# Performance work log

Measured on AMD Instinct MI355X. Metric: run time of the kernel, lower is better.

Reference implementation:

```python
import jax, jax.numpy as jnp
import numpy as np

B, H, T, K = 4, 32, 2048, 64
V = K


def setup_inputs() -> dict:
    key = jax.random.key(0)
    k1, k2, k3, k4, k5 = jax.random.split(key, 5)
    r = jax.random.normal(k1, (B, H, T, K), dtype=jnp.float32)
    k = jax.random.normal(k2, (B, H, T, K), dtype=jnp.float32)
    v = jax.random.normal(k3, (B, H, T, V), dtype=jnp.float32)
    # w is a log-decay; keep it negative so exp(w) in (0,1) and the T-step
    # recurrence is stable (matches real RWKV-6 decay values)
    w = -2.0 * jax.random.uniform(k4, (B, H, T, K), dtype=jnp.float32)
    u = jax.random.normal(k5, (H, K), dtype=jnp.float32)
    initial_state = jnp.zeros((B, H, K, V), dtype=jnp.float32)
    return {"r": r, "k": k, "v": v, "w": w, "u": u, "initial_state": initial_state}


def _rwkv6_scan(r, k, v, w, u, initial_state):
    scale = 1.0
    q = r * scale
    decay = jnp.exp(w)  # [B,H,T,K], matches torch: b_w = exp(w)

    # time-major for scan: [T,B,H,K]
    qT = jnp.moveaxis(q, 2, 0)
    kT = jnp.moveaxis(k, 2, 0)
    vT = jnp.moveaxis(v, 2, 0)
    wT = jnp.moveaxis(decay, 2, 0)

    u_b = u[None, :, :, None]  # [1,H,K,1] broadcast like torch b_u

    def step(h, inp):
        bq, bk, bv, bw = inp  # each [B,H,K] (bv is [B,H,V])
        kv = bk[..., :, None] * bv[..., None, :]          # [B,H,K,V]
        o = jnp.einsum('bhkv,bhk->bhv', h + kv * u_b, bq)  # sum over K
        h = h * bw[..., None] + kv                         # decay-gated update
        return h, o

    final_state, oT = jax.lax.scan(step, initial_state, (qT, kT, vT, wT))
    o = jnp.moveaxis(oT, 0, 2)  # [B,H,T,V]
    return o, final_state


def reference(r, k, v, w, u, initial_state):
    return _rwkv6_scan(r, k, v, w, u, initial_state)
```

## Files before the change

kernel.cpp:

```cpp
#include <hip/hip_runtime.h>
#include <math.h>


#define Bdim 4
#define Hdim 32
#define Tdim 2048
#define Kdim 64
#define Vdim 64
#define NC   32
#define CL   64
#define LP   72

typedef __attribute__((ext_vector_type(8))) short short8;
typedef __attribute__((ext_vector_type(4))) short short4_;
typedef __attribute__((ext_vector_type(4))) float float4_;

__device__ __forceinline__ short f2bf(float x) {
    unsigned u = __float_as_uint(x);
    unsigned r = (u + 0x7FFFu + ((u >> 16) & 1u)) >> 16;
    return (short)r;
}

#define MFMA(a, b, c) __builtin_amdgcn_mfma_f32_16x16x32_bf16(a, b, c, 0, 0, 0)

__device__ __forceinline__ void wg_barrier() {
    __builtin_amdgcn_sched_barrier(0);
    asm volatile("s_waitcnt lgkmcnt(0)");
    __builtin_amdgcn_s_barrier();
    __builtin_amdgcn_sched_barrier(0);
}

__global__ __launch_bounds__(512) void rwkv6_fused(
    const float* __restrict__ rin, const float* __restrict__ kin,
    const float* __restrict__ vin, const float* __restrict__ win,
    const float* __restrict__ uin, const float* __restrict__ init,
    float* __restrict__ oout, float* __restrict__ fin)
{
    __shared__ __attribute__((aligned(16))) short Qh[CL * LP];
    __shared__ __attribute__((aligned(16))) short Kh[CL * LP];
    __shared__ __attribute__((aligned(16))) short KhT[CL * LP];
    __shared__ __attribute__((aligned(16))) short Qt[CL * LP];
    __shared__ __attribute__((aligned(16))) short Am[CL * LP];
    __shared__ __attribute__((aligned(16))) short Vt[32 * LP];
    __shared__ __attribute__((aligned(16))) short Ht[32 * LP];
    __shared__ float bsum[8 * 64];
    __shared__ float Dd[CL];

    const int tid  = threadIdx.x;
    const int wv   = tid >> 6;
    const int lane = tid & 63;
    const int quad = lane >> 4, r = lane & 15;

    const int bid = blockIdx.x;
    const int vh  = bid >> 7;
    const int bh  = bid & 127;
    const int h_idx = bh & (Hdim - 1);

    const int m_s = wv >> 2;
    const int n_s = wv & 3;
    const int k_  = 16 * n_s + r;
    const int i_o = wv >> 1;
    const int n_o = wv & 1;

    const float u_ = uin[h_idx * Kdim + lane];

    const int svrow = tid & 31;
    const int skq   = tid >> 5;

    auto blk_addr = [](const short* buf, int row, int blk) -> const char* {
        const int phys = blk ^ ((row >> 3) & 3);
        return (const char*)buf + row * 144 + phys * 16;
    };

    for (int i = tid; i < CL * LP; i += 512) Am[i] = 0;

    float h[4];
#pragma unroll
    for (int reg = 0; reg < 4; ++reg) {
        const int vloc = 16 * m_s + quad * 4 + reg;
        h[reg] = init[((size_t)bh * Kdim + k_) * Vdim + 32 * vh + vloc];
        const int hb = ((k_ >> 3) ^ ((vloc >> 3) & 3));
        *(short*)((char*)Ht + vloc * 144 + hb * 16 + (k_ & 7) * 2) = f2bf(h[reg]);
    }

    float wl[8], ql[8], kl[8], vls[4];
    {
        const size_t b0 = (size_t)bh * Tdim * Kdim;
#pragma unroll
        for (int tt = 0; tt < 8; ++tt) wl[tt] = win[b0 + (8 * wv + tt) * Kdim + lane];
#pragma unroll
        for (int i = 0; i < 4; ++i)
            vls[i] = vin[b0 + (4 * skq + i) * Kdim + 32 * vh + svrow];
#pragma unroll
        for (int tt = 0; tt < 8; ++tt) ql[tt] = rin[b0 + (8 * wv + tt) * Kdim + lane];
#pragma unroll
        for (int tt = 0; tt < 8; ++tt) kl[tt] = kin[b0 + (8 * wv + tt) * Kdim + lane];
    }

    auto atile = [&](int i, int j) {
        const int trow = 16 * i + r;
        short8 qa0 = *(const short8*)&Qh[trow * LP + quad * 8];
        short8 qa1 = *(const short8*)&Qh[trow * LP + 32 + quad * 8];
        const int srow = 16 * j + r;
        const int sb = (srow >> 3) & 7;
        short8 kb0 = *(const short8*)&Kh[srow * LP + ((quad ^ sb) << 3)];
        short8 kb1 = *(const short8*)&Kh[srow * LP + (((quad + 4) ^ sb) << 3)];
        float4_ acc = {0.f, 0.f, 0.f, 0.f};
        acc = MFMA(qa0, kb0, acc);
        acc = MFMA(qa1, kb1, acc);
#pragma unroll
        for (int reg = 0; reg < 4; ++reg) {
            const int tg = 16 * i + quad * 4 + reg;
            const float val = (tg > srow) ? acc[reg] : ((tg == srow) ? Dd[tg] : 0.f);
            Am[tg * LP + srow] = f2bf(val);
        }
    };

    for (int c = 0; c < NC; ++c) {
        const size_t base = ((size_t)bh * Tdim + (size_t)c * CL) * Kdim;

        float wreg[8];
        float cwl = 0.f;
#pragma unroll
        for (int tt = 0; tt < 8; ++tt) { wreg[tt] = wl[tt]; cwl += wl[tt]; }
        bsum[wv * 64 + lane] = cwl;
        {
            short4_ pack;
#pragma unroll
            for (int i = 0; i < 4; ++i) pack[i] = f2bf(vls[i]);
            const int vb = ((skq >> 1) ^ ((svrow >> 3) & 3));
            *(short4_*)((char*)Vt + svrow * 144 + vb * 16 + (skq & 1) * 8) = pack;
        }
        wg_barrier();

        float b[8];
#pragma unroll
        for (int j = 0; j < 8; ++j) b[j] = bsum[j * 64 + lane];
        float pref = 0.f;
#pragma unroll
        for (int j = 0; j < 8; ++j) if (j < wv) pref += b[j];
        const float Cmid = b[0] + b[1] + b[2] + b[3];
        const float eC = __expf(Cmid);
        float cwrun = pref;
        short8 khrow;
#pragma unroll
        for (int tt = 0; tt < 8; ++tt) {
            const int t = 8 * wv + tt;
            const float cwp = cwrun;
            cwrun += wreg[tt];
            const float e1 = __expf(cwp - Cmid);
            Qh[t * LP + lane] = f2bf(ql[tt] * e1);
            Qt[t * LP + lane] = f2bf(ql[tt] * e1 * eC);
            const float e2 = __expf(Cmid - cwrun);
            const short kv = f2bf(kl[tt] * e2);
            Kh[t * LP + ((((lane >> 3) ^ ((t >> 3) & 7)) << 3) | (lane & 7))] = kv;
            khrow[tt] = kv;
            float d3 = ql[tt] * u_ * kl[tt];
#pragma unroll
            for (int off = 32; off > 0; off >>= 1) d3 += __shfl_xor(d3, off);
            if (lane == 0) Dd[t] = d3;
        }
        {
            const int kb = (wv ^ ((lane >> 3) & 3));
            *(short8*)((char*)KhT + lane * 144 + kb * 16) = khrow;
        }
        if (c + 1 < NC) {
            const size_t nb = base + (size_t)CL * Kdim;
#pragma unroll
            for (int tt = 0; tt < 8; ++tt) wl[tt] = win[nb + (8 * wv + tt) * Kdim + lane];
#pragma unroll
            for (int i = 0; i < 4; ++i)
                vls[i] = vin[nb + (4 * skq + i) * Kdim + 32 * vh + svrow];
#pragma unroll
            for (int tt = 0; tt < 8; ++tt) ql[tt] = rin[nb + (8 * wv + tt) * Kdim + lane];
#pragma unroll
            for (int tt = 0; tt < 8; ++tt) kl[tt] = kin[nb + (8 * wv + tt) * Kdim + lane];
        }
        wg_barrier();

        {
            int i0, j0;
            if (wv == 0)      { i0 = 0; j0 = 0; }
            else if (wv < 3)  { i0 = 1; j0 = wv - 1; }
            else if (wv < 6)  { i0 = 2; j0 = wv - 3; }
            else              { i0 = 3; j0 = wv - 6; }
            atile(i0, j0);
            if (wv < 2) atile(3, 2 + wv);
        }
        wg_barrier();

        {
            const int trow = 16 * i_o + r;
            short8 aa0 = *(const short8*)&Am[trow * LP + quad * 8];
            short8 aa1 = *(const short8*)&Am[trow * LP + 32 + quad * 8];
            short8 qt0 = *(const short8*)&Qt[trow * LP + quad * 8];
            short8 qt1 = *(const short8*)&Qt[trow * LP + 32 + quad * 8];
            const int vrow = 16 * n_o + r;
            short8 vb0 = *(const short8*)blk_addr(Vt, vrow, quad);
            short8 vb1 = *(const short8*)blk_addr(Vt, vrow, quad + 4);
            short8 hb0 = *(const short8*)blk_addr(Ht, vrow, quad);
            short8 hb1 = *(const short8*)blk_addr(Ht, vrow, quad + 4);
            float4_ o4 = {0.f, 0.f, 0.f, 0.f};
            o4 = MFMA(aa0, vb0, o4);
            o4 = MFMA(aa1, vb1, o4);
            o4 = MFMA(qt0, hb0, o4);
            o4 = MFMA(qt1, hb1, o4);
            float* op = oout + base;
#pragma unroll
            for (int reg = 0; reg < 4; ++reg)
                op[(16 * i_o + quad * 4 + reg) * Vdim + 32 * vh + 16 * n_o + r] = o4[reg];
        }

        float4_ sc = {0.f, 0.f, 0.f, 0.f};
        {
            const int vrow = 16 * m_s + r;
            short8 va0 = *(const short8*)blk_addr(Vt, vrow, quad);
            short8 va1 = *(const short8*)blk_addr(Vt, vrow, quad + 4);
            short8 kc0 = *(const short8*)blk_addr(KhT, k_, quad);
            short8 kc1 = *(const short8*)blk_addr(KhT, k_, quad + 4);
            sc = MFMA(va0, kc0, sc);
            sc = MFMA(va1, kc1, sc);
        }
        float totk = 0.f, cmk = 0.f;
#pragma unroll
        for (int j = 0; j < 8; ++j) {
            const float bb = bsum[j * 64 + k_];
            totk += bb;
            if (j < 4) cmk += bb;
        }
        wg_barrier();

        {
            const float eA = __expf(totk);
            const float eS = __expf(totk - cmk);
#pragma unroll
            for (int reg = 0; reg < 4; ++reg) {
                h[reg] = h[reg] * eA + sc[reg] * eS;
                const int vloc = 16 * m_s + quad * 4 + reg;
                const int hb = ((k_ >> 3) ^ ((vloc >> 3) & 3));
                *(short*)((char*)Ht + vloc * 144 + hb * 16 + (k_ & 7) * 2) = f2bf(h[reg]);
            }
        }
    }

#pragma unroll
    for (int reg = 0; reg < 4; ++reg)
        fin[((size_t)bh * Kdim + k_) * Vdim + 32 * vh + 16 * m_s + quad * 4 + reg] = h[reg];
}

extern "C" void kernel_launch(void* const* d_in, const int* in_sizes, int n_in,
                              void* d_out, int out_size, void* d_ws, size_t ws_size,
                              hipStream_t stream) {
    const float* r    = (const float*)d_in[0];
    const float* k    = (const float*)d_in[1];
    const float* v    = (const float*)d_in[2];
    const float* w    = (const float*)d_in[3];
    const float* u    = (const float*)d_in[4];
    const float* init = (const float*)d_in[5];

    float* o   = (float*)d_out;
    float* fin = o + (size_t)Bdim * Hdim * Tdim * Vdim;

    (void)d_ws; (void)ws_size;
    rwkv6_fused<<<Bdim * Hdim * 2, 512, 0, stream>>>(r, k, v, w, u, init, o, fin);
}
```

Before: 303.5 us.

## Split V into quarters across 512 blocks and specialize waves for output vs state

Each block now handles a 16-wide V slice instead of 32, doubling the grid to 512 workgroups so more CUs are busy. Waves 0-3 compute outputs while waves 4-7 compute the state update, and launch bounds request 4 blocks per CU. The per-row diagonal shuffle reduction is batched across 8 timesteps, and the XOR-swizzled LDS layouts are replaced by plain padded layouts. In exchange, the chunk-local attention matrix and the r/k/w loads and their exponentials are recomputed by twice as many blocks, and removing the swizzles may bring back LDS bank conflicts.

```diff
diff --git a/kernel.cpp b/kernel.cpp
--- a/kernel.cpp
+++ b/kernel.cpp
@@ -12,7 +12,6 @@
 #define LP   72
 
 typedef __attribute__((ext_vector_type(8))) short short8;
-typedef __attribute__((ext_vector_type(4))) short short4_;
 typedef __attribute__((ext_vector_type(4))) float float4_;
 
 __device__ __forceinline__ short f2bf(float x) {
@@ -30,7 +29,7 @@
     __builtin_amdgcn_sched_barrier(0);
 }
 
-__global__ __launch_bounds__(512) void rwkv6_fused(
+__global__ __launch_bounds__(512, 4) void rwkv6_fused(
     const float* __restrict__ rin, const float* __restrict__ kin,
     const float* __restrict__ vin, const float* __restrict__ win,
     const float* __restrict__ uin, const float* __restrict__ init,
@@ -41,8 +40,8 @@
     __shared__ __attribute__((aligned(16))) short KhT[CL * LP];
     __shared__ __attribute__((aligned(16))) short Qt[CL * LP];
     __shared__ __attribute__((aligned(16))) short Am[CL * LP];
-    __shared__ __attribute__((aligned(16))) short Vt[32 * LP];
-    __shared__ __attribute__((aligned(16))) short Ht[32 * LP];
+    __shared__ __attribute__((aligned(16))) short Vt[16 * LP];
+    __shared__ __attribute__((aligned(16))) short Ht[16 * LP];
     __shared__ float bsum[8 * 64];
     __shared__ float Dd[CL];
 
@@ -52,45 +51,37 @@
     const int quad = lane >> 4, r = lane & 15;
 
     const int bid = blockIdx.x;
-    const int vh  = bid >> 7;
+    const int vq  = bid >> 7;
     const int bh  = bid & 127;
     const int h_idx = bh & (Hdim - 1);
 
-    const int m_s = wv >> 2;
-    const int n_s = wv & 3;
-    const int k_  = 16 * n_s + r;
-    const int i_o = wv >> 1;
-    const int n_o = wv & 1;
+    const int k_  = 16 * (wv & 3) + r;
 
     const float u_ = uin[h_idx * Kdim + lane];
 
-    const int svrow = tid & 31;
-    const int skq   = tid >> 5;
-
-    auto blk_addr = [](const short* buf, int row, int blk) -> const char* {
-        const int phys = blk ^ ((row >> 3) & 3);
-        return (const char*)buf + row * 144 + phys * 16;
-    };
+    const int svrow = tid & 15;
+    const int st2   = tid >> 4;
 
     for (int i = tid; i < CL * LP; i += 512) Am[i] = 0;
 
-    float h[4];
-#pragma unroll
-    for (int reg = 0; reg < 4; ++reg) {
-        const int vloc = 16 * m_s + quad * 4 + reg;
-        h[reg] = init[((size_t)bh * Kdim + k_) * Vdim + 32 * vh + vloc];
-        const int hb = ((k_ >> 3) ^ ((vloc >> 3) & 3));
-        *(short*)((char*)Ht + vloc * 144 + hb * 16 + (k_ & 7) * 2) = f2bf(h[reg]);
-    }
-
-    float wl[8], ql[8], kl[8], vls[4];
+    float h[4] = {0.f, 0.f, 0.f, 0.f};
+    if (wv >= 4) {
+#pragma unroll
+        for (int reg = 0; reg < 4; ++reg) {
+            const int vloc = quad * 4 + reg;
+            h[reg] = init[((size_t)bh * Kdim + k_) * Vdim + 16 * vq + vloc];
+            Ht[vloc * LP + k_] = f2bf(h[reg]);
+        }
+    }
+
+    float wl[8], ql[8], kl[8], vls[2];
     {
         const size_t b0 = (size_t)bh * Tdim * Kdim;
 #pragma unroll
         for (int tt = 0; tt < 8; ++tt) wl[tt] = win[b0 + (8 * wv + tt) * Kdim + lane];
 #pragma unroll
-        for (int i = 0; i < 4; ++i)
-            vls[i] = vin[b0 + (4 * skq + i) * Kdim + 32 * vh + svrow];
+        for (int i = 0; i < 2; ++i)
+            vls[i] = vin[b0 + (2 * st2 + i) * Kdim + 16 * vq + svrow];
 #pragma unroll
         for (int tt = 0; tt < 8; ++tt) ql[tt] = rin[b0 + (8 * wv + tt) * Kdim + lane];
 #pragma unroll
@@ -102,9 +93,8 @@
         short8 qa0 = *(const short8*)&Qh[trow * LP + quad * 8];
         short8 qa1 = *(const short8*)&Qh[trow * LP + 32 + quad * 8];
         const int srow = 16 * j + r;
-        const int sb = (srow >> 3) & 7;
-        short8 kb0 = *(const short8*)&Kh[srow * LP + ((quad ^ sb) << 3)];
-        short8 kb1 = *(const short8*)&Kh[srow * LP + (((quad + 4) ^ sb) << 3)];
+        short8 kb0 = *(const short8*)&Kh[srow * LP + quad * 8];
+        short8 kb1 = *(const short8*)&Kh[srow * LP + 32 + quad * 8];
         float4_ acc = {0.f, 0.f, 0.f, 0.f};
         acc = MFMA(qa0, kb0, acc);
         acc = MFMA(qa1, kb1, acc);
@@ -116,6 +106,9 @@
         }
     };
 
+    float4_ sc;
+    float totk = 0.f, cmk = 0.f;
+
     for (int c = 0; c < NC; ++c) {
         const size_t base = ((size_t)bh * Tdim + (size_t)c * CL) * Kdim;
 
@@ -125,11 +118,9 @@
         for (int tt = 0; tt < 8; ++tt) { wreg[tt] = wl[tt]; cwl += wl[tt]; }
         bsum[wv * 64 + lane] = cwl;
         {
-            short4_ pack;
-#pragma unroll
-            for (int i = 0; i < 4; ++i) pack[i] = f2bf(vls[i]);
-            const int vb = ((skq >> 1) ^ ((svrow >> 3) & 3));
-            *(short4_*)((char*)Vt + svrow * 144 + vb * 16 + (skq & 1) * 8) = pack;
+            const unsigned p0 = (unsigned short)f2bf(vls[0]);
+            const unsigned p1 = (unsigned short)f2bf(vls[1]);
+            *(unsigned*)&Vt[svrow * LP + st2 * 2] = p0 | (p1 << 16);
         }
         wg_barrier();
 
@@ -143,6 +134,7 @@
         const float eC = __expf(Cmid);
         float cwrun = pref;
         short8 khrow;
+        float d3p[8];
 #pragma unroll
         for (int tt = 0; tt < 8; ++tt) {
             const int t = 8 * wv + tt;
@@ -153,24 +145,27 @@
             Qt[t * LP + lane] = f2bf(ql[tt] * e1 * eC);
             const float e2 = __expf(Cmid - cwrun);
             const short kv = f2bf(kl[tt] * e2);
-            Kh[t * LP + ((((lane >> 3) ^ ((t >> 3) & 7)) << 3) | (lane & 7))] = kv;
+            Kh[t * LP + lane] = kv;
             khrow[tt] = kv;
-            float d3 = ql[tt] * u_ * kl[tt];
-#pragma unroll
-            for (int off = 32; off > 0; off >>= 1) d3 += __shfl_xor(d3, off);
-            if (lane == 0) Dd[t] = d3;
-        }
-        {
-            const int kb = (wv ^ ((lane >> 3) & 3));
-            *(short8*)((char*)KhT + lane * 144 + kb * 16) = khrow;
+            d3p[tt] = ql[tt] * u_ * kl[tt];
+        }
+        *(short8*)&KhT[lane * LP + wv * 8] = khrow;
+#pragma unroll
+        for (int off = 32; off > 0; off >>= 1) {
+#pragma unroll
+            for (int tt = 0; tt < 8; ++tt) d3p[tt] += __shfl_xor(d3p[tt], off);
+        }
+        if (lane == 0) {
+#pragma unroll
+            for (int tt = 0; tt < 8; ++tt) Dd[8 * wv + tt] = d3p[tt];
         }
         if (c + 1 < NC) {
             const size_t nb = base + (size_t)CL * Kdim;
 #pragma unroll
             for (int tt = 0; tt < 8; ++tt) wl[tt] = win[nb + (8 * wv + tt) * Kdim + lane];
 #pragma unroll
-            for (int i = 0; i < 4; ++i)
-                vls[i] = vin[nb + (4 * skq + i) * Kdim + 32 * vh + svrow];
+            for (int i = 0; i < 2; ++i)
+                vls[i] = vin[nb + (2 * st2 + i) * Kdim + 16 * vq + svrow];
 #pragma unroll
             for (int tt = 0; tt < 8; ++tt) ql[tt] = rin[nb + (8 * wv + tt) * Kdim + lane];
 #pragma unroll
@@ -189,17 +184,16 @@
         }
         wg_barrier();
 
-        {
-            const int trow = 16 * i_o + r;
+        if (wv < 4) {
+            const int trow = 16 * wv + r;
             short8 aa0 = *(const short8*)&Am[trow * LP + quad * 8];
             short8 aa1 = *(const short8*)&Am[trow * LP + 32 + quad * 8];
             short8 qt0 = *(const short8*)&Qt[trow * LP + quad * 8];
             short8 qt1 = *(const short8*)&Qt[trow * LP + 32 + quad * 8];
-            const int vrow = 16 * n_o + r;
-            short8 vb0 = *(const short8*)blk_addr(Vt, vrow, quad);
-            short8 vb1 = *(const short8*)blk_addr(Vt, vrow, quad + 4);
-            short8 hb0 = *(const short8*)blk_addr(Ht, vrow, quad);
-            short8 hb1 = *(const short8*)blk_addr(Ht, vrow, quad + 4);
+            short8 vb0 = *(const short8*)&Vt[r * LP + quad * 8];
+            short8 vb1 = *(const short8*)&Vt[r * LP + 32 + quad * 8];
+            short8 hb0 = *(const short8*)&Ht[r * LP + quad * 8];
+            short8 hb1 = *(const short8*)&Ht[r * LP + 32 + quad * 8];
             float4_ o4 = {0.f, 0.f, 0.f, 0.f};
             o4 = MFMA(aa0, vb0, o4);
             o4 = MFMA(aa1, vb1, o4);
@@ -208,44 +202,41 @@
             float* op = oout + base;
 #pragma unroll
             for (int reg = 0; reg < 4; ++reg)
-                op[(16 * i_o + quad * 4 + reg) * Vdim + 32 * vh + 16 * n_o + r] = o4[reg];
-        }
-
-        float4_ sc = {0.f, 0.f, 0.f, 0.f};
-        {
-            const int vrow = 16 * m_s + r;
-            short8 va0 = *(const short8*)blk_addr(Vt, vrow, quad);
-            short8 va1 = *(const short8*)blk_addr(Vt, vrow, quad + 4);
-            short8 kc0 = *(const short8*)blk_addr(KhT, k_, quad);
-            short8 kc1 = *(const short8*)blk_addr(KhT, k_, quad + 4);
+                op[(16 * wv + quad * 4 + reg) * Vdim + 16 * vq + r] = o4[reg];
+        } else {
+            short8 va0 = *(const short8*)&Vt[r * LP + quad * 8];
+            short8 va1 = *(const short8*)&Vt[r * LP + 32 + quad * 8];
+            short8 kc0 = *(const short8*)&KhT[k_ * LP + quad * 8];
+            short8 kc1 = *(const short8*)&KhT[k_ * LP + 32 + quad * 8];
+            sc = (float4_){0.f, 0.f, 0.f, 0.f};
             sc = MFMA(va0, kc0, sc);
             sc = MFMA(va1, kc1, sc);
-        }
-        float totk = 0.f, cmk = 0.f;
-#pragma unroll
-        for (int j = 0; j < 8; ++j) {
-            const float bb = bsum[j * 64 + k_];
-            totk += bb;
-            if (j < 4) cmk += bb;
-        }
-        wg_barrier();
-
-        {
+            totk = 0.f; cmk = 0.f;
+#pragma unroll
+            for (int j = 0; j < 8; ++j) {
+                const float bb = bsum[j * 64 + k_];
+                totk += bb;
+                if (j < 4) cmk += bb;
+            }
+        }
+        wg_barrier();
+
+        if (wv >= 4) {
             const float eA = __expf(totk);
             const float eS = __expf(totk - cmk);
 #pragma unroll
             for (int reg = 0; reg < 4; ++reg) {
                 h[reg] = h[reg] * eA + sc[reg] * eS;
-                const int vloc = 16 * m_s + quad * 4 + reg;
-                const int hb = ((k_ >> 3) ^ ((vloc >> 3) & 3));
-                *(short*)((char*)Ht + vloc * 144 + hb * 16 + (k_ & 7) * 2) = f2bf(h[reg]);
+                Ht[(quad * 4 + reg) * LP + k_] = f2bf(h[reg]);
             }
         }
     }
 
-#pragma unroll
-    for (int reg = 0; reg < 4; ++reg)
-        fin[((size_t)bh * Kdim + k_) * Vdim + 32 * vh + 16 * m_s + quad * 4 + reg] = h[reg];
+    if (wv >= 4) {
+#pragma unroll
+        for (int reg = 0; reg < 4; ++reg)
+            fin[((size_t)bh * Kdim + k_) * Vdim + 16 * vq + quad * 4 + reg] = h[reg];
+    }
 }
 
 extern "C" void kernel_launch(void* const* d_in, const int* in_sizes, int n_in,
@@ -262,5 +253,5 @@
     float* fin = o + (size_t)Bdim * Hdim * Tdim * Vdim;
 
     (void)d_ws; (void)ws_size;
-    rwkv6_fused<<<Bdim * Hdim * 2, 512, 0, stream>>>(r, k, v, w, u, init, o, fin);
-}
+    rwkv6_fused<<<Bdim * Hdim * 4, 512, 0, stream>>>(r, k, v, w, u, init, o, fin);
+}
```

Result: slower. 361.5 us (+19.1%).

## Software-pipeline chunk preprocessing with double-buffered LDS and fewer barriers

Applied to the files above, without the earlier changes.

Double-buffers the Qh, KhT, Vt, Ht and bsum tiles so the decay-scaled Q/K preparation for chunk c+1 overlaps the MFMA work of chunk c. This cuts the per-chunk barriers from four to two, and prefetching moves two chunks ahead. It also folds the exp(Cmid) scaling into the bf16 state copy, which removes the separate Qt buffer. The wave reductions are batched, s_setprio is raised around the MFMA sections, and the XOR swizzles are dropped, which could bring back LDS bank conflicts.

```diff
diff --git a/kernel.cpp b/kernel.cpp
--- a/kernel.cpp
+++ b/kernel.cpp
@@ -36,14 +36,13 @@
     const float* __restrict__ uin, const float* __restrict__ init,
     float* __restrict__ oout, float* __restrict__ fin)
 {
-    __shared__ __attribute__((aligned(16))) short Qh[CL * LP];
+    __shared__ __attribute__((aligned(16))) short Qh[2][CL * LP];
     __shared__ __attribute__((aligned(16))) short Kh[CL * LP];
-    __shared__ __attribute__((aligned(16))) short KhT[CL * LP];
-    __shared__ __attribute__((aligned(16))) short Qt[CL * LP];
+    __shared__ __attribute__((aligned(16))) short KhT[2][CL * LP];
     __shared__ __attribute__((aligned(16))) short Am[CL * LP];
-    __shared__ __attribute__((aligned(16))) short Vt[32 * LP];
-    __shared__ __attribute__((aligned(16))) short Ht[32 * LP];
-    __shared__ float bsum[8 * 64];
+    __shared__ __attribute__((aligned(16))) short Vt[2][32 * LP];
+    __shared__ __attribute__((aligned(16))) short Ht[2][32 * LP];
+    __shared__ float bsum[2][8 * 64];
     __shared__ float Dd[CL];
 
     const int tid  = threadIdx.x;
@@ -67,44 +66,74 @@
     const int svrow = tid & 31;
     const int skq   = tid >> 5;
 
-    auto blk_addr = [](const short* buf, int row, int blk) -> const char* {
-        const int phys = blk ^ ((row >> 3) & 3);
-        return (const char*)buf + row * 144 + phys * 16;
-    };
-
     for (int i = tid; i < CL * LP; i += 512) Am[i] = 0;
 
-    float h[4];
-#pragma unroll
-    for (int reg = 0; reg < 4; ++reg) {
-        const int vloc = 16 * m_s + quad * 4 + reg;
-        h[reg] = init[((size_t)bh * Kdim + k_) * Vdim + 32 * vh + vloc];
-        const int hb = ((k_ >> 3) ^ ((vloc >> 3) & 3));
-        *(short*)((char*)Ht + vloc * 144 + hb * 16 + (k_ & 7) * 2) = f2bf(h[reg]);
-    }
-
     float wl[8], ql[8], kl[8], vls[4];
-    {
-        const size_t b0 = (size_t)bh * Tdim * Kdim;
-#pragma unroll
-        for (int tt = 0; tt < 8; ++tt) wl[tt] = win[b0 + (8 * wv + tt) * Kdim + lane];
+
+    auto do_prefetch = [&](size_t nb) {
+#pragma unroll
+        for (int tt = 0; tt < 8; ++tt) wl[tt] = win[nb + (8 * wv + tt) * Kdim + lane];
 #pragma unroll
         for (int i = 0; i < 4; ++i)
-            vls[i] = vin[b0 + (4 * skq + i) * Kdim + 32 * vh + svrow];
-#pragma unroll
-        for (int tt = 0; tt < 8; ++tt) ql[tt] = rin[b0 + (8 * wv + tt) * Kdim + lane];
-#pragma unroll
-        for (int tt = 0; tt < 8; ++tt) kl[tt] = kin[b0 + (8 * wv + tt) * Kdim + lane];
-    }
-
-    auto atile = [&](int i, int j) {
+            vls[i] = vin[nb + (4 * skq + i) * Kdim + 32 * vh + svrow];
+#pragma unroll
+        for (int tt = 0; tt < 8; ++tt) ql[tt] = rin[nb + (8 * wv + tt) * Kdim + lane];
+#pragma unroll
+        for (int tt = 0; tt < 8; ++tt) kl[tt] = kin[nb + (8 * wv + tt) * Kdim + lane];
+    };
+
+    auto do_pass1 = [&](int Y) {
+        float cwl = 0.f;
+#pragma unroll
+        for (int tt = 0; tt < 8; ++tt) cwl += wl[tt];
+        bsum[Y][wv * 64 + lane] = cwl;
+        short4_ pack;
+#pragma unroll
+        for (int i = 0; i < 4; ++i) pack[i] = f2bf(vls[i]);
+        *(short4_*)&Vt[Y][svrow * LP + 4 * skq] = pack;
+    };
+
+    auto do_pass2 = [&](int Y) {
+        float b8[8];
+#pragma unroll
+        for (int j = 0; j < 8; ++j) b8[j] = bsum[Y][j * 64 + lane];
+        float pref = 0.f;
+#pragma unroll
+        for (int j = 0; j < 8; ++j) if (j < wv) pref += b8[j];
+        const float Cmid = b8[0] + b8[1] + b8[2] + b8[3];
+        float cwrun = pref;
+        short8 khrow;
+        float d3p[8];
+#pragma unroll
+        for (int tt = 0; tt < 8; ++tt) {
+            const int t = 8 * wv + tt;
+            const float cwp = cwrun;
+            cwrun += wl[tt];
+            Qh[Y][t * LP + lane] = f2bf(ql[tt] * __expf(cwp - Cmid));
+            const short kv = f2bf(kl[tt] * __expf(Cmid - cwrun));
+            Kh[t * LP + lane] = kv;
+            khrow[tt] = kv;
+            d3p[tt] = ql[tt] * u_ * kl[tt];
+        }
+        *(short8*)&KhT[Y][lane * LP + wv * 8] = khrow;
+#pragma unroll
+        for (int off = 32; off > 0; off >>= 1) {
+#pragma unroll
+            for (int tt = 0; tt < 8; ++tt) d3p[tt] += __shfl_xor(d3p[tt], off);
+        }
+        if (lane == 0) {
+#pragma unroll
+            for (int tt = 0; tt < 8; ++tt) Dd[8 * wv + tt] = d3p[tt];
+        }
+    };
+
+    auto atile = [&](int X, int i, int j) {
         const int trow = 16 * i + r;
-        short8 qa0 = *(const short8*)&Qh[trow * LP + quad * 8];
-        short8 qa1 = *(const short8*)&Qh[trow * LP + 32 + quad * 8];
+        short8 qa0 = *(const short8*)&Qh[X][trow * LP + quad * 8];
+        short8 qa1 = *(const short8*)&Qh[X][trow * LP + 32 + quad * 8];
         const int srow = 16 * j + r;
-        const int sb = (srow >> 3) & 7;
-        short8 kb0 = *(const short8*)&Kh[srow * LP + ((quad ^ sb) << 3)];
-        short8 kb1 = *(const short8*)&Kh[srow * LP + (((quad + 4) ^ sb) << 3)];
+        short8 kb0 = *(const short8*)&Kh[srow * LP + quad * 8];
+        short8 kb1 = *(const short8*)&Kh[srow * LP + 32 + quad * 8];
         float4_ acc = {0.f, 0.f, 0.f, 0.f};
         acc = MFMA(qa0, kb0, acc);
         acc = MFMA(qa1, kb1, acc);
@@ -116,131 +145,104 @@
         }
     };
 
+    const size_t bh_base = (size_t)bh * Tdim * Kdim;
+    do_prefetch(bh_base);
+    do_pass1(0);
+    wg_barrier();
+    do_pass2(0);
+    float h[4];
+    {
+        const float cm0 = bsum[0][0 * 64 + k_] + bsum[0][64 + k_]
+                        + bsum[0][128 + k_] + bsum[0][192 + k_];
+        const float eH = __expf(cm0);
+#pragma unroll
+        for (int reg = 0; reg < 4; ++reg) {
+            const int vloc = 16 * m_s + quad * 4 + reg;
+            h[reg] = init[((size_t)bh * Kdim + k_) * Vdim + 32 * vh + vloc];
+            Ht[0][vloc * LP + k_] = f2bf(h[reg] * eH);
+        }
+    }
+    do_prefetch(bh_base + (size_t)CL * Kdim);
+    wg_barrier();
+
     for (int c = 0; c < NC; ++c) {
-        const size_t base = ((size_t)bh * Tdim + (size_t)c * CL) * Kdim;
-
-        float wreg[8];
-        float cwl = 0.f;
-#pragma unroll
-        for (int tt = 0; tt < 8; ++tt) { wreg[tt] = wl[tt]; cwl += wl[tt]; }
-        bsum[wv * 64 + lane] = cwl;
-        {
-            short4_ pack;
-#pragma unroll
-            for (int i = 0; i < 4; ++i) pack[i] = f2bf(vls[i]);
-            const int vb = ((skq >> 1) ^ ((svrow >> 3) & 3));
-            *(short4_*)((char*)Vt + svrow * 144 + vb * 16 + (skq & 1) * 8) = pack;
-        }
-        wg_barrier();
-
-        float b[8];
-#pragma unroll
-        for (int j = 0; j < 8; ++j) b[j] = bsum[j * 64 + lane];
-        float pref = 0.f;
-#pragma unroll
-        for (int j = 0; j < 8; ++j) if (j < wv) pref += b[j];
-        const float Cmid = b[0] + b[1] + b[2] + b[3];
-        const float eC = __expf(Cmid);
-        float cwrun = pref;
-        short8 khrow;
-#pragma unroll
-        for (int tt = 0; tt < 8; ++tt) {
-            const int t = 8 * wv + tt;
-            const float cwp = cwrun;
-            cwrun += wreg[tt];
-            const float e1 = __expf(cwp - Cmid);
-            Qh[t * LP + lane] = f2bf(ql[tt] * e1);
-            Qt[t * LP + lane] = f2bf(ql[tt] * e1 * eC);
-            const float e2 = __expf(Cmid - cwrun);
-            const short kv = f2bf(kl[tt] * e2);
-            Kh[t * LP + ((((lane >> 3) ^ ((t >> 3) & 7)) << 3) | (lane & 7))] = kv;
-            khrow[tt] = kv;
-            float d3 = ql[tt] * u_ * kl[tt];
-#pragma unroll
-            for (int off = 32; off > 0; off >>= 1) d3 += __shfl_xor(d3, off);
-            if (lane == 0) Dd[t] = d3;
-        }
-        {
-            const int kb = (wv ^ ((lane >> 3) & 3));
-            *(short8*)((char*)KhT + lane * 144 + kb * 16) = khrow;
-        }
-        if (c + 1 < NC) {
-            const size_t nb = base + (size_t)CL * Kdim;
-#pragma unroll
-            for (int tt = 0; tt < 8; ++tt) wl[tt] = win[nb + (8 * wv + tt) * Kdim + lane];
-#pragma unroll
-            for (int i = 0; i < 4; ++i)
-                vls[i] = vin[nb + (4 * skq + i) * Kdim + 32 * vh + svrow];
-#pragma unroll
-            for (int tt = 0; tt < 8; ++tt) ql[tt] = rin[nb + (8 * wv + tt) * Kdim + lane];
-#pragma unroll
-            for (int tt = 0; tt < 8; ++tt) kl[tt] = kin[nb + (8 * wv + tt) * Kdim + lane];
-        }
-        wg_barrier();
-
+        const int X = c & 1, Y = X ^ 1;
+        const size_t base = bh_base + (size_t)c * CL * Kdim;
+
+        if (c + 1 < NC) do_pass1(Y);
+        __builtin_amdgcn_s_setprio(1);
         {
             int i0, j0;
             if (wv == 0)      { i0 = 0; j0 = 0; }
             else if (wv < 3)  { i0 = 1; j0 = wv - 1; }
             else if (wv < 6)  { i0 = 2; j0 = wv - 3; }
             else              { i0 = 3; j0 = wv - 6; }
-            atile(i0, j0);
-            if (wv < 2) atile(3, 2 + wv);
-        }
+            atile(X, i0, j0);
+            if (wv < 2) atile(X, 3, 2 + wv);
+        }
+        __builtin_amdgcn_s_setprio(0);
         wg_barrier();
 
+        if (c + 1 < NC) do_pass2(Y);
+        if (c + 2 < NC) do_prefetch(bh_base + (size_t)(c + 2) * CL * Kdim);
+
+        __builtin_amdgcn_s_setprio(1);
         {
             const int trow = 16 * i_o + r;
             short8 aa0 = *(const short8*)&Am[trow * LP + quad * 8];
             short8 aa1 = *(const short8*)&Am[trow * LP + 32 + quad * 8];
-            short8 qt0 = *(const short8*)&Qt[trow * LP + quad * 8];
-            short8 qt1 = *(const short8*)&Qt[trow * LP + 32 + quad * 8];
+            short8 qh0 = *(const short8*)&Qh[X][trow * LP + quad * 8];
+            short8 qh1 = *(const short8*)&Qh[X][trow * LP + 32 + quad * 8];
             const int vrow = 16 * n_o + r;
-            short8 vb0 = *(const short8*)blk_addr(Vt, vrow, quad);
-            short8 vb1 = *(const short8*)blk_addr(Vt, vrow, quad + 4);
-            short8 hb0 = *(const short8*)blk_addr(Ht, vrow, quad);
-            short8 hb1 = *(const short8*)blk_addr(Ht, vrow, quad + 4);
+            short8 vb0 = *(const short8*)&Vt[X][vrow * LP + quad * 8];
+            short8 vb1 = *(const short8*)&Vt[X][vrow * LP + 32 + quad * 8];
+            short8 hb0 = *(const short8*)&Ht[X][vrow * LP + quad * 8];
+            short8 hb1 = *(const short8*)&Ht[X][vrow * LP + 32 + quad * 8];
             float4_ o4 = {0.f, 0.f, 0.f, 0.f};
             o4 = MFMA(aa0, vb0, o4);
             o4 = MFMA(aa1, vb1, o4);
-            o4 = MFMA(qt0, hb0, o4);
-            o4 = MFMA(qt1, hb1, o4);
+            o4 = MFMA(qh0, hb0, o4);
+            o4 = MFMA(qh1, hb1, o4);
             float* op = oout + base;
 #pragma unroll
             for (int reg = 0; reg < 4; ++reg)
                 op[(16 * i_o + quad * 4 + reg) * Vdim + 32 * vh + 16 * n_o + r] = o4[reg];
         }
-
         float4_ sc = {0.f, 0.f, 0.f, 0.f};
         {
             const int vrow = 16 * m_s + r;
-            short8 va0 = *(const short8*)blk_addr(Vt, vrow, quad);
-            short8 va1 = *(const short8*)blk_addr(Vt, vrow, quad + 4);
-            short8 kc0 = *(const short8*)blk_addr(KhT, k_, quad);
-            short8 kc1 = *(const short8*)blk_addr(KhT, k_, quad + 4);
+            short8 va0 = *(const short8*)&Vt[X][vrow * LP + quad * 8];
+            short8 va1 = *(const short8*)&Vt[X][vrow * LP + 32 + quad * 8];
+            short8 kc0 = *(const short8*)&KhT[X][k_ * LP + quad * 8];
+            short8 kc1 = *(const short8*)&KhT[X][k_ * LP + 32 + quad * 8];
             sc = MFMA(va0, kc0, sc);
             sc = MFMA(va1, kc1, sc);
         }
-        float totk = 0.f, cmk = 0.f;
-#pragma unroll
-        for (int j = 0; j < 8; ++j) {
-            const float bb = bsum[j * 64 + k_];
-            totk += bb;
-            if (j < 4) cmk += bb;
-        }
-        wg_barrier();
-
-        {
+        __builtin_amdgcn_s_setprio(0);
+
+        {
+            float totk = 0.f, cmk = 0.f;
+#pragma unroll
+            for (int j = 0; j < 8; ++j) {
+                const float bb = bsum[X][j * 64 + k_];
+                totk += bb;
+                if (j < 4) cmk += bb;
+            }
             const float eA = __expf(totk);
             const float eS = __expf(totk - cmk);
 #pragma unroll
-            for (int reg = 0; reg < 4; ++reg) {
+            for (int reg = 0; reg < 4; ++reg)
                 h[reg] = h[reg] * eA + sc[reg] * eS;
-                const int vloc = 16 * m_s + quad * 4 + reg;
-                const int hb = ((k_ >> 3) ^ ((vloc >> 3) & 3));
-                *(short*)((char*)Ht + vloc * 144 + hb * 16 + (k_ & 7) * 2) = f2bf(h[reg]);
+            if (c + 1 < NC) {
+                const float cm1 = bsum[Y][0 * 64 + k_] + bsum[Y][64 + k_]
+                                + bsum[Y][128 + k_] + bsum[Y][192 + k_];
+                const float eH = __expf(cm1);
+#pragma unroll
+                for (int reg = 0; reg < 4; ++reg)
+                    Ht[Y][(16 * m_s + quad * 4 + reg) * LP + k_] = f2bf(h[reg] * eH);
             }
         }
+        wg_barrier();
     }
 
 #pragma unroll
```

Result: faster. 292.4 us (-3.6%).
